# Kernel optimization log

Measured on AMD Instinct MI355X. Metric: run time of the kernel, lower is better.

The kernel has to match this reference:

```python
import jax, jax.numpy as jnp
import numpy as np

B, T, D_IN, D_HID, TAG = 32, 2048, 1024, 2048, 2

def setup_inputs() -> dict:
    key = jax.random.key(0)
    k1, k2, k3, k4, k5, k6 = jax.random.split(key, 6)
    h = jax.random.normal(k1, (B, T, D_IN), dtype=jnp.float32)
    # valid lengths in [1, T] (avoid zero-length divide)
    text_len = jnp.maximum(jax.random.randint(k2, (B,), 0, T), 1)
    s1 = 1.0 / np.sqrt(D_IN)
    s2 = 1.0 / np.sqrt(D_HID)
    W1 = jax.random.uniform(k3, (D_HID, D_IN), minval=-s1, maxval=s1, dtype=jnp.float32)
    b1 = jax.random.uniform(k4, (D_HID,), minval=-s1, maxval=s1, dtype=jnp.float32)
    W2 = jax.random.uniform(k5, (TAG, D_HID), minval=-s2, maxval=s2, dtype=jnp.float32)
    b2 = jax.random.uniform(k6, (TAG,), minval=-s2, maxval=s2, dtype=jnp.float32)
    return {"h": h, "text_len": text_len, "W1": W1, "b1": b1, "W2": W2, "b2": b2}

def reference(h, text_len, W1, b1, W2, b2):
    # lin1 + relu (dropout is identity at inference)
    hidden = jax.nn.relu(jnp.einsum('btd,hd->bth', h, W1) + b1)  # [B,T,H]
    # masked mean over the first text_len[i] positions per sample
    mask = (jnp.arange(hidden.shape[1])[None, :] < text_len[:, None]).astype(hidden.dtype)  # [B,T]
    pooled = jnp.einsum('bth,bt->bh', hidden, mask) / text_len[:, None].astype(hidden.dtype)  # [B,H]
    score = jnp.einsum('bh,th->bt', pooled, W2) + b2  # [B,TAG]
    return score
```

## Files before the change

kernel.cpp:

```cpp
#include <hip/hip_runtime.h>
#include <hip/hip_bf16.h>

#define B_   32
#define T_   2048
#define DIN  1024
#define DHID 2048
#define TAG  2

#define BM   256
#define BN   256
#define BK   64
#define NT   (DIN / BK)

typedef __attribute__((ext_vector_type(8))) short bf16x8;
typedef __attribute__((ext_vector_type(4))) float f32x4;
typedef __attribute__((ext_vector_type(4))) int   i32x4;

union BF8 { bf16x8 v; i32x4 i; unsigned int u[4]; };

__device__ inline unsigned int f2bf_u(float f) {
    unsigned int u = __float_as_uint(f);
    return (u + 0x7FFFu + ((u >> 16) & 1u)) >> 16;
}
__device__ inline unsigned int pack2bf(float a, float b) {
    return f2bf_u(a) | (f2bf_u(b) << 16);
}

#define BARRIER()  asm volatile("s_barrier" ::: "memory")
#define LGKM0()    asm volatile("s_waitcnt lgkmcnt(0)" ::: "memory")
#define VMCNT(n)   asm volatile("s_waitcnt vmcnt(" #n ")" ::: "memory")

__global__ void convert_w1(const float* __restrict__ W1,
                           unsigned short* __restrict__ W1b,
                           float* __restrict__ pooled) {
    int idx = blockIdx.x * blockDim.x + threadIdx.x;
    float4 f = ((const float4*)W1)[idx];
    ((uint2*)W1b)[idx] = uint2{pack2bf(f.x, f.y), pack2bf(f.z, f.w)};
    if (idx < B_ * DHID / 4) ((float4*)pooled)[idx] = float4{0.f, 0.f, 0.f, 0.f};
}

__global__ void convert_h(const float* __restrict__ h,
                          const int*   __restrict__ text_len,
                          unsigned short* __restrict__ hb) {
    const int b   = blockIdx.y;
    const int idx = blockIdx.x * 256 + threadIdx.x;
    const int t   = idx >> 7;
    if (t >= text_len[b]) return;
    const size_t gi = (size_t)b * (T_ * DIN / 8) + idx;
    float4 f0 = ((const float4*)h)[gi * 2];
    float4 f1 = ((const float4*)h)[gi * 2 + 1];
    uint4 o;
    o.x = pack2bf(f0.x, f0.y);
    o.y = pack2bf(f0.z, f0.w);
    o.z = pack2bf(f1.x, f1.y);
    o.w = pack2bf(f1.z, f1.w);
    ((uint4*)hb)[gi] = o;
}

__global__ __launch_bounds__(512, 2) void scorer_gemm_8ph(
    const unsigned short* __restrict__ hb,
    const int*            __restrict__ text_len,
    const unsigned short* __restrict__ W1b,
    const float*          __restrict__ b1,
    float*                __restrict__ pooled) {

    const int nt  = blockIdx.x;
    const int tt  = blockIdx.y;
    const int b   = blockIdx.z;
    const int len = text_len[b];
    const int t0  = tt * BM;
    if (t0 >= len) return;
    const int n0  = nt * BN;

    __shared__ __align__(16) unsigned short lds[4 * BM * BK];

    const int tid  = threadIdx.x;
    const int lane = tid & 63;
    const int wid  = tid >> 6;
    const int wm   = wid >> 2;
    const int wn   = wid & 3;
    const int quad = lane >> 4;
    const int l15  = lane & 15;

    const int srow   = lane >> 3;
    const int schunk = (lane & 7) ^ srow;
    const unsigned short* gA = hb  + ((size_t)b * T_ + t0 + wid * 8 + srow) * DIN + schunk * 8;
    const unsigned short* gB = W1b + ((size_t)(n0 + wid * 8 + srow)) * DIN + schunk * 8;
    const int sdst = wid * 512;

    auto stageA = [&](int d, int h, int k0) {
#pragma unroll
        for (int i = 0; i < 2; ++i) {
            const unsigned short* gp = gA + (size_t)(h * 128 + i * 64) * DIN + k0;
            __builtin_amdgcn_global_load_lds(
                (const __attribute__((address_space(1))) void*)gp,
                (__attribute__((address_space(3))) void*)(lds + d * 16384 + (h * 128 + i * 64) * 64 + sdst),
                16, 0, 0);
        }
    };
    auto stageB = [&](int d, int h, int k0) {
#pragma unroll
        for (int i = 0; i < 2; ++i) {
            const unsigned short* gp = gB + (size_t)(h * 128 + i * 64) * DIN + k0;
            __builtin_amdgcn_global_load_lds(
                (const __attribute__((address_space(1))) void*)gp,
                (__attribute__((address_space(3))) void*)(lds + 32768 + d * 16384 + (h * 128 + i * 64) * 64 + sdst),
                16, 0, 0);
        }
    };

    auto rdA = [&](const unsigned short* As, int mi, int ks) -> i32x4 {
        int row  = (mi >> 2) * 128 + wm * 64 + (mi & 3) * 16 + l15;
        int slot = (ks * 4 + quad) ^ (l15 & 7);
        return *(const i32x4*)(As + row * 64 + slot * 8);
    };
    auto rdB = [&](const unsigned short* Bs, int ni, int ks) -> i32x4 {
        int row  = (ni >> 1) * 128 + wn * 32 + (ni & 1) * 16 + l15;
        int slot = (ks * 4 + quad) ^ (l15 & 7);
        return *(const i32x4*)(Bs + row * 64 + slot * 8);
    };

    f32x4 acc[8][4] = {};
    BF8 a[4][2], bb[4][2];

    stageA(0, 0, 0);  stageB(0, 0, 0);  stageB(0, 1, 0);  stageA(0, 1, 0);
    stageA(1, 0, BK); stageB(1, 0, BK); stageB(1, 1, BK);
    VMCNT(6);
    BARRIER();

    for (int t = 0; t < NT; ++t) {
        const int k0 = t * BK;
        const unsigned short* As = lds + (t & 1) * 16384;
        const unsigned short* Bs = lds + 32768 + (t & 1) * 16384;

#pragma unroll
        for (int mi = 0; mi < 4; ++mi)
#pragma unroll
            for (int ks = 0; ks < 2; ++ks)
                a[mi][ks].i = rdA(As, mi, ks);
#pragma unroll
        for (int ni = 0; ni < 2; ++ni)
#pragma unroll
            for (int ks = 0; ks < 2; ++ks)
                bb[ni][ks].i = rdB(Bs, ni, ks);
        if (t + 1 < NT) stageA((t + 1) & 1, 1, k0 + BK);
        BARRIER();
        LGKM0();
        __builtin_amdgcn_s_setprio(1);
#pragma unroll
        for (int mi = 0; mi < 4; ++mi)
#pragma unroll
            for (int ni = 0; ni < 2; ++ni)
#pragma unroll
                for (int ks = 0; ks < 2; ++ks)
                    acc[mi][ni] = __builtin_amdgcn_mfma_f32_16x16x32_bf16(
                        a[mi][ks].v, bb[ni][ks].v, acc[mi][ni], 0, 0, 0);
        __builtin_amdgcn_s_setprio(0);
        BARRIER();

#pragma unroll
        for (int ni = 2; ni < 4; ++ni)
#pragma unroll
            for (int ks = 0; ks < 2; ++ks)
                bb[ni][ks].i = rdB(Bs, ni, ks);
        if (t + 2 < NT) stageA(t & 1, 0, k0 + 2 * BK);
        BARRIER();
        LGKM0();
        __builtin_amdgcn_s_setprio(1);
#pragma unroll
        for (int mi = 0; mi < 4; ++mi)
#pragma unroll
            for (int ni = 2; ni < 4; ++ni)
#pragma unroll
                for (int ks = 0; ks < 2; ++ks)
                    acc[mi][ni] = __builtin_amdgcn_mfma_f32_16x16x32_bf16(
                        a[mi][ks].v, bb[ni][ks].v, acc[mi][ni], 0, 0, 0);
        __builtin_amdgcn_s_setprio(0);
        BARRIER();

#pragma unroll
        for (int mi = 0; mi < 4; ++mi)
#pragma unroll
            for (int ks = 0; ks < 2; ++ks)
                a[mi][ks].i = rdA(As, mi + 4, ks);
        if (t + 2 < NT) stageB(t & 1, 0, k0 + 2 * BK);
        BARRIER();
        LGKM0();
        __builtin_amdgcn_s_setprio(1);
#pragma unroll
        for (int mi = 0; mi < 4; ++mi)
#pragma unroll
            for (int ni = 2; ni < 4; ++ni)
#pragma unroll
                for (int ks = 0; ks < 2; ++ks)
                    acc[4 + mi][ni] = __builtin_amdgcn_mfma_f32_16x16x32_bf16(
                        a[mi][ks].v, bb[ni][ks].v, acc[4 + mi][ni], 0, 0, 0);
        __builtin_amdgcn_s_setprio(0);
        BARRIER();

        if (t + 2 < NT) stageB(t & 1, 1, k0 + 2 * BK);
        if (t < NT - 2)       { VMCNT(6); }
        else if (t == NT - 2) { VMCNT(0); }
        BARRIER();
        __builtin_amdgcn_s_setprio(1);
#pragma unroll
        for (int mi = 0; mi < 4; ++mi)
#pragma unroll
            for (int ni = 0; ni < 2; ++ni)
#pragma unroll
                for (int ks = 0; ks < 2; ++ks)
                    acc[4 + mi][ni] = __builtin_amdgcn_mfma_f32_16x16x32_bf16(
                        a[mi][ks].v, bb[ni][ks].v, acc[4 + mi][ni], 0, 0, 0);
        __builtin_amdgcn_s_setprio(0);
        BARRIER();
    }

#pragma unroll
    for (int ni = 0; ni < 4; ++ni) {
        int n = n0 + (ni >> 1) * 128 + wn * 32 + (ni & 1) * 16 + l15;
        float bias = b1[n];
        float colsum = 0.f;
#pragma unroll
        for (int mi = 0; mi < 8; ++mi) {
            int trow = t0 + (mi >> 2) * 128 + wm * 64 + (mi & 3) * 16 + quad * 4;
#pragma unroll
            for (int r = 0; r < 4; ++r) {
                float v = acc[mi][ni][r] + bias;
                v = v > 0.f ? v : 0.f;
                if (trow + r < len) colsum += v;
            }
        }
        colsum += __shfl_xor(colsum, 16);
        colsum += __shfl_xor(colsum, 32);
        if (quad == 0) atomicAdd(&pooled[b * DHID + n], colsum);
    }
}

__global__ void scorer_gemm_direct(const float* __restrict__ hin,
                                   const int*   __restrict__ text_len,
                                   const unsigned short* __restrict__ W1b,
                                   const float* __restrict__ b1,
                                   float*       __restrict__ pooled) {
    const int tt  = blockIdx.x;
    const int b   = blockIdx.y;
    const int len = text_len[b];
    const int t0  = tt * 64;
    if (t0 >= len) return;
    const int tid = threadIdx.x, lane = tid & 63, wid = tid >> 6;
    const int wrow = wid >> 1, wcol = wid & 1, quad = lane >> 4, l15 = lane & 15;
    const float* aptr[2];
#pragma unroll
    for (int mi = 0; mi < 2; ++mi)
        aptr[mi] = hin + ((size_t)b * T_ + t0 + wrow * 32 + mi * 16 + l15) * DIN + quad * 8;
    for (int nout = 0; nout < DHID / 128; ++nout) {
        const int nbase = nout * 128;
        f32x4 acc[2][4] = {};
        const unsigned short* bptr[4];
        float b1v[4];
#pragma unroll
        for (int ni = 0; ni < 4; ++ni) {
            int n = nbase + wcol * 64 + ni * 16 + l15;
            bptr[ni] = W1b + (size_t)n * DIN + quad * 8;
            b1v[ni]  = b1[n];
        }
        for (int k = 0; k < DIN; k += 32) {
            BF8 a[2], w[4];
#pragma unroll
            for (int mi = 0; mi < 2; ++mi) {
                float4 f0 = *(const float4*)(aptr[mi] + k);
                float4 f1 = *(const float4*)(aptr[mi] + k + 4);
                a[mi].u[0] = pack2bf(f0.x, f0.y);
                a[mi].u[1] = pack2bf(f0.z, f0.w);
                a[mi].u[2] = pack2bf(f1.x, f1.y);
                a[mi].u[3] = pack2bf(f1.z, f1.w);
            }
#pragma unroll
            for (int ni = 0; ni < 4; ++ni) w[ni].i = *(const i32x4*)(bptr[ni] + k);
#pragma unroll
            for (int mi = 0; mi < 2; ++mi)
#pragma unroll
                for (int ni = 0; ni < 4; ++ni)
                    acc[mi][ni] = __builtin_amdgcn_mfma_f32_16x16x32_bf16(
                        a[mi].v, w[ni].v, acc[mi][ni], 0, 0, 0);
        }
#pragma unroll
        for (int ni = 0; ni < 4; ++ni) {
            float colsum = 0.f;
#pragma unroll
            for (int mi = 0; mi < 2; ++mi) {
                int trow = t0 + wrow * 32 + mi * 16 + quad * 4;
#pragma unroll
                for (int r = 0; r < 4; ++r) {
                    float v = acc[mi][ni][r] + b1v[ni];
                    v = v > 0.f ? v : 0.f;
                    if (trow + r < len) colsum += v;
                }
            }
            colsum += __shfl_xor(colsum, 16);
            colsum += __shfl_xor(colsum, 32);
            if (quad == 0)
                atomicAdd(&pooled[b * DHID + nbase + wcol * 64 + ni * 16 + l15], colsum);
        }
    }
}

__global__ void finalize_k(const float* __restrict__ pooled,
                           const int*   __restrict__ text_len,
                           const float* __restrict__ W2,
                           const float* __restrict__ b2,
                           float*       __restrict__ out) {
    int b = blockIdx.x, tid = threadIdx.x;
    float s0 = 0.f, s1 = 0.f;
    for (int hh = tid; hh < DHID; hh += 256) {
        float p = pooled[b * DHID + hh];
        s0 += p * W2[hh];
        s1 += p * W2[DHID + hh];
    }
#pragma unroll
    for (int off = 32; off > 0; off >>= 1) {
        s0 += __shfl_down(s0, off);
        s1 += __shfl_down(s1, off);
    }
    __shared__ float r0[4], r1[4];
    int wid = tid >> 6, lane = tid & 63;
    if (lane == 0) { r0[wid] = s0; r1[wid] = s1; }
    __syncthreads();
    if (tid == 0) {
        float inv = 1.0f / (float)text_len[b];
        out[b * 2 + 0] = (r0[0] + r0[1] + r0[2] + r0[3]) * inv + b2[0];
        out[b * 2 + 1] = (r1[0] + r1[1] + r1[2] + r1[3]) * inv + b2[1];
    }
}

extern "C" void kernel_launch(void* const* d_in, const int* in_sizes, int n_in,
                              void* d_out, int out_size, void* d_ws, size_t ws_size,
                              hipStream_t stream) {
    const float* hin      = (const float*)d_in[0];
    const int*   text_len = (const int*)  d_in[1];
    const float* W1       = (const float*)d_in[2];
    const float* b1       = (const float*)d_in[3];
    const float* W2       = (const float*)d_in[4];
    const float* b2       = (const float*)d_in[5];
    float* out = (float*)d_out;

    const size_t HB_BYTES  = (size_t)B_ * T_ * DIN * 2;
    const size_t W1B_BYTES = (size_t)DHID * DIN * 2;
    const size_t NEED      = HB_BYTES + W1B_BYTES + (size_t)B_ * DHID * 4;

    if (ws_size >= NEED) {
        unsigned short* hb     = (unsigned short*)d_ws;
        unsigned short* W1b    = (unsigned short*)((char*)d_ws + HB_BYTES);
        float*          pooled = (float*)((char*)d_ws + HB_BYTES + W1B_BYTES);

        convert_w1<<<(DHID * DIN / 4) / 256, 256, 0, stream>>>(W1, W1b, pooled);
        dim3 hgrid((T_ * DIN / 8) / 256, B_);
        convert_h<<<hgrid, 256, 0, stream>>>(hin, text_len, hb);

        dim3 grid(DHID / BN, T_ / BM, B_);
        scorer_gemm_8ph<<<grid, 512, 0, stream>>>(hb, text_len, W1b, b1, pooled);
        finalize_k<<<B_, 256, 0, stream>>>(pooled, text_len, W2, b2, out);
    } else {
        unsigned short* W1b    = (unsigned short*)d_ws;
        float*          pooled = (float*)((char*)d_ws + W1B_BYTES);
        (void)hipMemsetAsync(pooled, 0, B_ * DHID * sizeof(float), stream);
        convert_w1<<<(DHID * DIN / 4) / 256, 256, 0, stream>>>(W1, W1b, pooled);
        dim3 grid(T_ / 64, B_);
        scorer_gemm_direct<<<grid, 256, 0, stream>>>(hin, text_len, W1b, b1, pooled);
        finalize_k<<<B_, 256, 0, stream>>>(pooled, text_len, W2, b2, out);
    }
}
```

Measured before the change: 535.9 us.

## Fuse conversion kernels, remap GEMM block order, merge last pipeline phases

Merges the W1 and h bf16 conversion kernels into one launch with extra grid rows for W1, removing one kernel launch. The GEMM grid becomes a flat 1D index with a swizzled mapping that staggers batch index against the T tile, so early-exiting blocks and busy blocks spread across CUs and XCDs. It also issues both B stagings together and fuses the last two MFMA phases into one, cutting a barrier pair per k-step. The risk is less overlap between memory traffic and compute inside the loop.

```diff
diff --git a/kernel.cpp b/kernel.cpp
--- a/kernel.cpp
+++ b/kernel.cpp
@@ -39,9 +39,19 @@
     if (idx < B_ * DHID / 4) ((float4*)pooled)[idx] = float4{0.f, 0.f, 0.f, 0.f};
 }
 
-__global__ void convert_h(const float* __restrict__ h,
-                          const int*   __restrict__ text_len,
-                          unsigned short* __restrict__ hb) {
+__global__ void convert_all(const float* __restrict__ h,
+                            const int*   __restrict__ text_len,
+                            unsigned short* __restrict__ hb,
+                            const float* __restrict__ W1,
+                            unsigned short* __restrict__ W1b,
+                            float* __restrict__ pooled) {
+    if (blockIdx.y >= B_) {
+        int idx = ((blockIdx.y - B_) * 1024 + blockIdx.x) * 256 + threadIdx.x;
+        float4 f = ((const float4*)W1)[idx];
+        ((uint2*)W1b)[idx] = uint2{pack2bf(f.x, f.y), pack2bf(f.z, f.w)};
+        if (idx < B_ * DHID / 4) ((float4*)pooled)[idx] = float4{0.f, 0.f, 0.f, 0.f};
+        return;
+    }
     const int b   = blockIdx.y;
     const int idx = blockIdx.x * 256 + threadIdx.x;
     const int t   = idx >> 7;
@@ -64,9 +74,15 @@
     const float*          __restrict__ b1,
     float*                __restrict__ pooled) {
 
-    const int nt  = blockIdx.x;
-    const int tt  = blockIdx.y;
-    const int b   = blockIdx.z;
+    const int bid = blockIdx.x;
+    const int x   = bid & 7;
+    const int i   = bid >> 3;
+    const int nt  = i & 7;
+    const int m   = i >> 3;
+    const int tt  = m & 7;
+    const int bq  = m >> 3;
+    const int b   = ((x - tt) & 7) + (bq << 3);
+
     const int len = text_len[b];
     const int t0  = tt * BM;
     if (t0 >= len) return;
@@ -90,21 +106,21 @@
 
     auto stageA = [&](int d, int h, int k0) {
 #pragma unroll
-        for (int i = 0; i < 2; ++i) {
-            const unsigned short* gp = gA + (size_t)(h * 128 + i * 64) * DIN + k0;
+        for (int j = 0; j < 2; ++j) {
+            const unsigned short* gp = gA + (size_t)(h * 128 + j * 64) * DIN + k0;
             __builtin_amdgcn_global_load_lds(
                 (const __attribute__((address_space(1))) void*)gp,
-                (__attribute__((address_space(3))) void*)(lds + d * 16384 + (h * 128 + i * 64) * 64 + sdst),
+                (__attribute__((address_space(3))) void*)(lds + d * 16384 + (h * 128 + j * 64) * 64 + sdst),
                 16, 0, 0);
         }
     };
     auto stageB = [&](int d, int h, int k0) {
 #pragma unroll
-        for (int i = 0; i < 2; ++i) {
-            const unsigned short* gp = gB + (size_t)(h * 128 + i * 64) * DIN + k0;
+        for (int j = 0; j < 2; ++j) {
+            const unsigned short* gp = gB + (size_t)(h * 128 + j * 64) * DIN + k0;
             __builtin_amdgcn_global_load_lds(
                 (const __attribute__((address_space(1))) void*)gp,
-                (__attribute__((address_space(3))) void*)(lds + 32768 + d * 16384 + (h * 128 + i * 64) * 64 + sdst),
+                (__attribute__((address_space(3))) void*)(lds + 32768 + d * 16384 + (h * 128 + j * 64) * 64 + sdst),
                 16, 0, 0);
         }
     };
@@ -183,30 +199,19 @@
 #pragma unroll
             for (int ks = 0; ks < 2; ++ks)
                 a[mi][ks].i = rdA(As, mi + 4, ks);
-        if (t + 2 < NT) stageB(t & 1, 0, k0 + 2 * BK);
+        if (t + 2 < NT) {
+            stageB(t & 1, 0, k0 + 2 * BK);
+            stageB(t & 1, 1, k0 + 2 * BK);
+        }
+        if (t < NT - 2)       { VMCNT(6); }
+        else if (t == NT - 2) { VMCNT(0); }
         BARRIER();
         LGKM0();
         __builtin_amdgcn_s_setprio(1);
 #pragma unroll
         for (int mi = 0; mi < 4; ++mi)
 #pragma unroll
-            for (int ni = 2; ni < 4; ++ni)
-#pragma unroll
-                for (int ks = 0; ks < 2; ++ks)
-                    acc[4 + mi][ni] = __builtin_amdgcn_mfma_f32_16x16x32_bf16(
-                        a[mi][ks].v, bb[ni][ks].v, acc[4 + mi][ni], 0, 0, 0);
-        __builtin_amdgcn_s_setprio(0);
-        BARRIER();
-
-        if (t + 2 < NT) stageB(t & 1, 1, k0 + 2 * BK);
-        if (t < NT - 2)       { VMCNT(6); }
-        else if (t == NT - 2) { VMCNT(0); }
-        BARRIER();
-        __builtin_amdgcn_s_setprio(1);
-#pragma unroll
-        for (int mi = 0; mi < 4; ++mi)
-#pragma unroll
-            for (int ni = 0; ni < 2; ++ni)
+            for (int ni = 0; ni < 4; ++ni)
 #pragma unroll
                 for (int ks = 0; ks < 2; ++ks)
                     acc[4 + mi][ni] = __builtin_amdgcn_mfma_f32_16x16x32_bf16(
@@ -352,12 +357,10 @@
         unsigned short* W1b    = (unsigned short*)((char*)d_ws + HB_BYTES);
         float*          pooled = (float*)((char*)d_ws + HB_BYTES + W1B_BYTES);
 
-        convert_w1<<<(DHID * DIN / 4) / 256, 256, 0, stream>>>(W1, W1b, pooled);
-        dim3 hgrid((T_ * DIN / 8) / 256, B_);
-        convert_h<<<hgrid, 256, 0, stream>>>(hin, text_len, hb);
-
-        dim3 grid(DHID / BN, T_ / BM, B_);
-        scorer_gemm_8ph<<<grid, 512, 0, stream>>>(hb, text_len, W1b, b1, pooled);
+        dim3 cgrid(1024, B_ + 2);
+        convert_all<<<cgrid, 256, 0, stream>>>(hin, text_len, hb, W1, W1b, pooled);
+
+        scorer_gemm_8ph<<<2048, 512, 0, stream>>>(hb, text_len, W1b, b1, pooled);
         finalize_k<<<B_, 256, 0, stream>>>(pooled, text_len, W2, b2, out);
     } else {
         unsigned short* W1b    = (unsigned short*)d_ws;
```

New measurement: 508.1 us. -5.2%, faster.
